# Kernel tuning notes

Hardware: AMD Instinct MI355X
Metric: run time of the kernel (lower is better)

Reference implementation:

```python
import jax, jax.numpy as jnp
import numpy as np


def _hilbert_envelope(x1d):
    """|analytic signal| of a real 1-D signal, matching scipy.signal.hilbert."""
    N = x1d.shape[0]  # static at trace time
    h = np.zeros(N, dtype=np.float32)
    if N % 2 == 0:
        h[0] = 1.0
        h[N // 2] = 1.0
        h[1:N // 2] = 2.0
    else:
        h[0] = 1.0
        h[1:(N + 1) // 2] = 2.0
    Xf = jnp.fft.fft(x1d)
    analytic = jnp.fft.ifft(Xf * jnp.asarray(h))
    return jnp.abs(analytic)


def setup_inputs() -> dict:
    key = jax.random.key(0)
    B, L, D = 32, 4096, 64
    x = jax.random.normal(key, (B, L, D), dtype=jnp.float32)
    return {"x": x}


def reference(x):
    B, L, D = x.shape
    flat = x.reshape(-1)  # [B*L*D], one long signal as in the original
    up = jnp.clip(flat, 0.0, None)
    down = jnp.clip(-flat, 0.0, None)
    envelope_max = _hilbert_envelope(up).reshape(B, L, D)
    envelope_min = (-_hilbert_envelope(down)).reshape(B, L, D)
    avg_envelope = (envelope_max + envelope_min) * 0.5
    imf = x - avg_envelope
    # torch.std(dim=1, unbiased=True) -> ddof=1 over the time axis
    std_res = jnp.std(imf, axis=1, keepdims=True, ddof=1) + jnp.float32(0.01)
    return imf / std_res, avg_envelope
```

## Files before the change

kernel.cpp:

```cpp
#include <hip/hip_runtime.h>
#include <math.h>

#define NTOT 8388608
#define N1   2048
#define N2   4096
#define BB   32
#define LL   4096
#define DD   64

enum { M_NONE = 0, M_TW = 1, M_SCALE = 4 };

__device__ inline float2 cmul(float2 a, float2 b) {
    return make_float2(a.x*b.x - a.y*b.y, a.x*b.y + a.y*b.x);
}
__device__ inline float2 cmul_conj(float2 a, float2 b) {
    return make_float2(a.x*b.x + a.y*b.y, a.y*b.x - a.x*b.y);
}
__device__ inline float2 cadd(float2 a, float2 b){ return make_float2(a.x+b.x, a.y+b.y); }
__device__ inline float2 csub(float2 a, float2 b){ return make_float2(a.x-b.x, a.y-b.y); }
__device__ inline float2 mul_pi(float2 a){ return make_float2(-a.y, a.x); }
__device__ inline float2 mul_mi(float2 a){ return make_float2(a.y, -a.x); }
__device__ inline int pidx(int a){ return a + (a >> 4); }

template<bool INV>
__device__ inline void dft8(const float2* x, float2* y) {
    const float C = 0.70710678118654752f;
    float2 t0=cadd(x[0],x[4]), t1=cadd(x[1],x[5]), t2=cadd(x[2],x[6]), t3=cadd(x[3],x[7]);
    float2 u0=csub(x[0],x[4]), u1=csub(x[1],x[5]), u2=csub(x[2],x[6]), u3=csub(x[3],x[7]);
    if (!INV) {
        u1 = make_float2(C*(u1.x+u1.y), C*(u1.y-u1.x));
        u2 = mul_mi(u2);
        u3 = make_float2(C*(u3.y-u3.x), -C*(u3.x+u3.y));
    } else {
        u1 = make_float2(C*(u1.x-u1.y), C*(u1.y+u1.x));
        u2 = mul_pi(u2);
        u3 = make_float2(-C*(u3.x+u3.y), C*(u3.x-u3.y));
    }
    {
        float2 s0=cadd(t0,t2), s1=cadd(t1,t3), d0=csub(t0,t2);
        float2 d1 = INV ? mul_pi(csub(t1,t3)) : mul_mi(csub(t1,t3));
        y[0]=cadd(s0,s1); y[4]=csub(s0,s1); y[2]=cadd(d0,d1); y[6]=csub(d0,d1);
    }
    {
        float2 s0=cadd(u0,u2), s1=cadd(u1,u3), d0=csub(u0,u2);
        float2 d1 = INV ? mul_pi(csub(u1,u3)) : mul_mi(csub(u1,u3));
        y[1]=cadd(s0,s1); y[5]=csub(s0,s1); y[3]=cadd(d0,d1); y[7]=csub(d0,d1);
    }
}

template<bool INV>
__device__ inline void dft16(const float2* x, float2* y) {
    const float C  = 0.70710678118654752f;
    const float c1 = 0.92387953251128674f;
    const float s1 = 0.38268343236508977f;
    float2 e[8], o[8], E[8], O[8];
    #pragma unroll
    for (int m = 0; m < 8; ++m) { e[m] = x[2*m]; o[m] = x[2*m+1]; }
    dft8<INV>(e, E);
    dft8<INV>(o, O);
    O[1] = cmul(O[1], make_float2( c1, INV ?  s1 : -s1));
    O[2] = cmul(O[2], make_float2(  C, INV ?   C : -C ));
    O[3] = cmul(O[3], make_float2( s1, INV ?  c1 : -c1));
    O[4] = INV ? mul_pi(O[4]) : mul_mi(O[4]);
    O[5] = cmul(O[5], make_float2(-s1, INV ?  c1 : -c1));
    O[6] = cmul(O[6], make_float2( -C, INV ?   C : -C ));
    O[7] = cmul(O[7], make_float2(-c1, INV ?  s1 : -s1));
    #pragma unroll
    for (int k = 0; k < 8; ++k) {
        y[k]     = cadd(E[k], O[k]);
        y[k + 8] = csub(E[k], O[k]);
    }
}

__device__ inline void dft8_h0_inv(const float2* x, float2* y) {
    const float C = 0.70710678118654752f;
    float2 u1 = make_float2(C*(x[1].x - x[1].y), C*(x[1].y + x[1].x));
    float2 u2 = mul_pi(x[2]);
    float2 u3 = make_float2(-C*(x[3].x + x[3].y), C*(x[3].x - x[3].y));
    {
        float2 s0=cadd(x[0],x[2]), s1=cadd(x[1],x[3]), d0=csub(x[0],x[2]);
        float2 d1 = mul_pi(csub(x[1],x[3]));
        y[0]=cadd(s0,s1); y[4]=csub(s0,s1); y[2]=cadd(d0,d1); y[6]=csub(d0,d1);
    }
    {
        float2 s0=cadd(x[0],u2), s1=cadd(u1,u3), d0=csub(x[0],u2);
        float2 d1 = mul_pi(csub(u1,u3));
        y[1]=cadd(s0,s1); y[5]=csub(s0,s1); y[3]=cadd(d0,d1); y[7]=csub(d0,d1);
    }
}

template<bool INV>
__device__ inline void dft4(const float2* u, float2* y) {
    float2 s0=cadd(u[0],u[2]), s1=cadd(u[1],u[3]), d0=csub(u[0],u[2]);
    float2 d1 = INV ? mul_pi(csub(u[1],u[3])) : mul_mi(csub(u[1],u[3]));
    y[0]=cadd(s0,s1); y[2]=csub(s0,s1); y[1]=cadd(d0,d1); y[3]=csub(d0,d1);
}

template<bool INV, int SH>
__device__ inline void twiddle8(float2* y, int ps, const float2* __restrict__ T1t) {
    float2 w1 = T1t[(ps << SH) & 4095];
    float2 w2 = cmul(w1, w1);
    float2 w3 = cmul(w2, w1);
    float2 w4 = cmul(w2, w2);
    float2 w5 = cmul(w4, w1);
    float2 w6 = cmul(w3, w3);
    float2 w7 = cmul(w4, w3);
    if (!INV) {
        y[1]=cmul(y[1],w1); y[2]=cmul(y[2],w2); y[3]=cmul(y[3],w3);
        y[4]=cmul(y[4],w4); y[5]=cmul(y[5],w5); y[6]=cmul(y[6],w6); y[7]=cmul(y[7],w7);
    } else {
        y[1]=cmul_conj(y[1],w1); y[2]=cmul_conj(y[2],w2); y[3]=cmul_conj(y[3],w3);
        y[4]=cmul_conj(y[4],w4); y[5]=cmul_conj(y[5],w5); y[6]=cmul_conj(y[6],w6); y[7]=cmul_conj(y[7],w7);
    }
}

template<bool INV>
__device__ inline void twiddle16(float2* y, int ps, const float2* __restrict__ T1t) {
    float2 w[16];
    w[1] = T1t[ps & 4095];
    w[2] = cmul(w[1], w[1]);
    w[3] = cmul(w[2], w[1]);
    w[4] = cmul(w[2], w[2]);
    w[5] = cmul(w[4], w[1]);
    w[6] = cmul(w[3], w[3]);
    w[7] = cmul(w[4], w[3]);
    w[8] = cmul(w[4], w[4]);
    w[9] = cmul(w[8], w[1]);
    w[10]= cmul(w[5], w[5]);
    w[11]= cmul(w[8], w[3]);
    w[12]= cmul(w[6], w[6]);
    w[13]= cmul(w[8], w[5]);
    w[14]= cmul(w[7], w[7]);
    w[15]= cmul(w[8], w[7]);
    #pragma unroll
    for (int k = 1; k < 16; ++k)
        y[k] = INV ? cmul_conj(y[k], w[k]) : cmul(y[k], w[k]);
}

__device__ inline float2 wbig(int t, const float2* __restrict__ T1t, const float2* __restrict__ T2t) {
    return cmul(T1t[t >> 11], T2t[t & 2047]);
}

template<bool INV, int MODE>
__global__ __launch_bounds__(256) void fft4096(float2* data,
                                               const float2* __restrict__ T1t,
                                               const float2* __restrict__ T2t) {
    __shared__ float2 S[4352];
    const int t = threadIdx.x;
    const int r = blockIdx.x;
    float2* base = data + (size_t)r * 4096;

    float2 x[16], y[16];
    #pragma unroll
    for (int m = 0; m < 16; ++m) x[m] = base[t + 256*m];

    dft16<INV>(x, y);
    twiddle16<INV>(y, t, T1t);
    #pragma unroll
    for (int k = 0; k < 16; ++k) S[pidx(16*t + k)] = y[k];
    __syncthreads();
    #pragma unroll
    for (int m = 0; m < 16; ++m) x[m] = S[pidx(t + 256*m)];

    dft16<INV>(x, y);
    {
        const int q = t & 15, ps = t - q;
        twiddle16<INV>(y, ps, T1t);
        __syncthreads();
        #pragma unroll
        for (int k = 0; k < 16; ++k) S[pidx(16*ps + q + 16*k)] = y[k];
    }
    __syncthreads();
    #pragma unroll
    for (int m = 0; m < 16; ++m) x[m] = S[pidx(t + 256*m)];

    dft16<INV>(x, y);

    if (MODE == M_TW) {
        float2 wb    = wbig(r * t, T1t, T2t);
        float2 wstep = wbig(256 * r, T1t, T2t);
        #pragma unroll
        for (int k = 0; k < 16; ++k) {
            int o = t + 256*k;
            base[o] = INV ? cmul_conj(y[k], wb) : cmul(y[k], wb);
            wb = INV ? cmul_conj(wb, wstep) : cmul(wb, wstep);
        }
    } else {
        #pragma unroll
        for (int k = 0; k < 16; ++k) {
            int o = t + 256*k;
            float2 v = y[k];
            if (MODE == M_SCALE) {
                const float sc = 1.f / 8388608.f;
                v.x *= sc; v.y *= sc;
            }
            base[o] = v;
        }
    }
}

__global__ __launch_bounds__(256) void fftmid(float2* data,
                                              const float2* __restrict__ T1t,
                                              const float2* __restrict__ T2t) {
    __shared__ float2 S[2176];
    const int t = threadIdx.x;
    const int r = blockIdx.x;
    float2* base = data + (size_t)r * 2048;

    float2 x[8], y[8];
    #pragma unroll
    for (int m = 0; m < 8; ++m) x[m] = base[t + 256*m];

    #pragma unroll
    for (int st = 0; st < 3; ++st) {
        const int s = 1 << (3*st);
        const int q = t & (s - 1);
        const int ps = t - q;
        dft8<false>(x, y);
        twiddle8<false, 1>(y, ps, T1t);
        if (st) __syncthreads();
        #pragma unroll
        for (int k = 0; k < 8; ++k) S[pidx(8*ps + q + k*s)] = y[k];
        __syncthreads();
        if (st < 2) {
            #pragma unroll
            for (int m = 0; m < 8; ++m) x[m] = S[pidx(t + 256*m)];
        }
    }
    float2 xa[4], xb[4], ya[4], yb[4];
    #pragma unroll
    for (int m = 0; m < 4; ++m) {
        xa[m] = S[pidx(t + 512*m)];
        xb[m] = S[pidx(t + 256 + 512*m)];
    }
    dft4<false>(xa, ya);
    dft4<false>(xb, yb);
    {
        float2 z[4];
        float h0 = (t == 0 && r == 0) ? 1.f : 2.f;
        z[0] = make_float2(ya[0].x * h0, ya[0].y * h0);
        z[1] = make_float2(yb[0].x * 2.f, yb[0].y * 2.f);
        z[2] = make_float2(ya[1].x * 2.f, ya[1].y * 2.f);
        z[3] = make_float2(yb[1].x * 2.f, yb[1].y * 2.f);
        dft8_h0_inv(z, y);
        if (t == 0 && r == 0) {
            float2 c = ya[2];
            #pragma unroll
            for (int k = 0; k < 8; ++k) {
                if (k & 1) { y[k].x -= c.x; y[k].y -= c.y; }
                else       { y[k].x += c.x; y[k].y += c.y; }
            }
        }
    }
    twiddle8<true, 1>(y, t, T1t);
    __syncthreads();
    #pragma unroll
    for (int k = 0; k < 8; ++k) S[pidx(8*t + k)] = y[k];
    __syncthreads();
    #pragma unroll
    for (int st = 1; st < 3; ++st) {
        const int s = 1 << (3*st);
        const int q = t & (s - 1);
        const int ps = t - q;
        #pragma unroll
        for (int m = 0; m < 8; ++m) x[m] = S[pidx(t + 256*m)];
        dft8<true>(x, y);
        twiddle8<true, 1>(y, ps, T1t);
        __syncthreads();
        #pragma unroll
        for (int k = 0; k < 8; ++k) S[pidx(8*ps + q + k*s)] = y[k];
        __syncthreads();
    }
    #pragma unroll
    for (int m = 0; m < 4; ++m) {
        xa[m] = S[pidx(t + 512*m)];
        xb[m] = S[pidx(t + 256 + 512*m)];
    }
    dft4<true>(xa, ya);
    dft4<true>(xb, yb);
    {
        float2 wka   = wbig(r * t, T1t, T2t);
        float2 w256  = wbig(256 * r, T1t, T2t);
        float2 w512  = cmul(w256, w256);
        float2 wkb   = cmul(wka, w256);
        #pragma unroll
        for (int k = 0; k < 4; ++k) {
            int o = t + 512*k;
            base[o]       = cmul_conj(ya[k], wka);
            base[o + 256] = cmul_conj(yb[k], wkb);
            wka = cmul(wka, w512);
            wkb = cmul(wkb, w512);
        }
    }
}

__global__ __launch_bounds__(256) void k_pre(const float* __restrict__ x, float2* __restrict__ A,
                                             float2* T1, float2* T2) {
    __shared__ float tile[32][33];
    int c0 = blockIdx.x * 32;
    int r0 = blockIdx.y * 32;
    int tx = threadIdx.x, ty = threadIdx.y;
    if (blockIdx.y == 0 && blockIdx.x < 24) {
        int j = blockIdx.x * 256 + ty * 32 + tx;
        if (j < 4096) {
            double ang = -2.0 * M_PI * (double)j / 4096.0;
            T1[j] = make_float2((float)cos(ang), (float)sin(ang));
        } else if (j < 4096 + 2048) {
            int b = j - 4096;
            double ang = -2.0 * M_PI * (double)b / 8388608.0;
            T2[b] = make_float2((float)cos(ang), (float)sin(ang));
        }
    }
    #pragma unroll
    for (int j = 0; j < 32; j += 8)
        tile[ty + j][tx] = x[(size_t)(r0 + ty + j) * N1 + c0 + tx];
    __syncthreads();
    #pragma unroll
    for (int j = 0; j < 32; j += 8) {
        float v = tile[tx][ty + j];
        A[(size_t)(c0 + ty + j) * N2 + r0 + tx] = make_float2(fmaxf(v, 0.f), fmaxf(-v, 0.f));
    }
}

__global__ __launch_bounds__(256) void k_trans(const float2* __restrict__ in, float2* __restrict__ out,
                                               int inCols, int inRows) {
    __shared__ float2 tile[32][33];
    int c0 = blockIdx.x * 32;
    int r0 = blockIdx.y * 32;
    int tx = threadIdx.x, ty = threadIdx.y;
    #pragma unroll
    for (int j = 0; j < 32; j += 8)
        tile[ty + j][tx] = in[(size_t)(r0 + ty + j) * inCols + c0 + tx];
    __syncthreads();
    #pragma unroll
    for (int j = 0; j < 32; j += 8)
        out[(size_t)(c0 + ty + j) * inRows + r0 + tx] = tile[tx][ty + j];
}

__global__ __launch_bounds__(256) void k_post(const float2* __restrict__ A, const float* __restrict__ x,
                                              float* __restrict__ out, float* __restrict__ part) {
    __shared__ float2 tile[32][33];
    __shared__ float red[2][8][32];
    int c0 = blockIdx.x * 32;
    int r0 = blockIdx.y * 32;
    int tx = threadIdx.x, ty = threadIdx.y;
    #pragma unroll
    for (int j = 0; j < 32; j += 8)
        tile[ty + j][tx] = A[(size_t)(r0 + ty + j) * N2 + c0 + tx];
    __syncthreads();
    float s1 = 0.f, s2 = 0.f;
    #pragma unroll
    for (int j = 0; j < 32; j += 8) {
        int n2 = c0 + ty + j;
        int n1 = r0 + tx;
        size_t n = (size_t)n2 * N1 + n1;
        float2 w = tile[tx][ty + j];
        float xv = x[n];
        float up = fmaxf(xv, 0.f);
        float dn = fmaxf(-xv, 0.f);
        float hu = w.y - dn;
        float hd = up - w.x;
        float em = sqrtf(up*up + hu*hu);
        float en = sqrtf(dn*dn + hd*hd);
        float avg = 0.5f * (em - en);
        float imf = xv - avg;
        out[NTOT + n] = avg;
        s1 += imf;
        s2 += imf * imf;
    }
    red[0][ty][tx] = s1;
    red[1][ty][tx] = s2;
    __syncthreads();
    if (ty == 0) {
        #pragma unroll
        for (int e = 1; e < 8; ++e) { s1 += red[0][e][tx]; s2 += red[1][e][tx]; }
        int slot = blockIdx.y * 128 + blockIdx.x;
        part[slot * 32 + tx]          = s1;
        part[262144 + slot * 32 + tx] = s2;
    }
}

__global__ __launch_bounds__(256) void std_final(const float* __restrict__ part, float* __restrict__ scalev) {
    int g = blockIdx.x * 256 + threadIdx.x;
    int b = g >> 6, d = g & 63;
    int dh = d >> 5, dl = d & 31;
    float s1 = 0.f, s2 = 0.f;
    for (int lq = 0; lq < 32; ++lq) {
        int by = lq * 2 + dh;
        #pragma unroll
        for (int ch = 0; ch < 4; ++ch) {
            int slot = by * 128 + b * 4 + ch;
            s1 += part[slot * 32 + dl];
            s2 += part[262144 + slot * 32 + dl];
        }
    }
    float mean = s1 / (float)LL;
    float var  = (s2 - (float)LL * mean * mean) / (float)(LL - 1);
    var = fmaxf(var, 0.f);
    scalev[g] = 1.f / (sqrtf(var) + 0.01f);
}

__global__ __launch_bounds__(256) void imf_final(const float* __restrict__ x, float* __restrict__ out,
                                                 const float* __restrict__ scalev) {
    size_t i = ((size_t)blockIdx.x * 256 + threadIdx.x) * 4;
    float4 xv = *(const float4*)(x + i);
    float4 av = *(const float4*)(out + NTOT + i);
    int b = (int)(i >> 18);
    int d = (int)(i & 63);
    const float* sc = scalev + b * 64;
    float4 v;
    v.x = (xv.x - av.x) * sc[d];
    v.y = (xv.y - av.y) * sc[d + 1];
    v.z = (xv.z - av.z) * sc[d + 2];
    v.w = (xv.w - av.w) * sc[d + 3];
    *(float4*)(out + i) = v;
}

extern "C" void kernel_launch(void* const* d_in, const int* in_sizes, int n_in,
                              void* d_out, int out_size, void* d_ws, size_t ws_size,
                              hipStream_t stream) {
    const float* x = (const float*)d_in[0];
    float* out = (float*)d_out;
    char* w = (char*)d_ws;

    float2* T1     = (float2*)w;
    float2* T2     = (float2*)(w + 32 * 1024);
    float*  scalev = (float*)(w + 48 * 1024);
    float2* A      = (float2*)(w + (1 << 20));
    float2* Bbuf   = (float2*)d_out;
    float*  part   = (float*)d_out;

    hipLaunchKernelGGL(k_pre, dim3(N1/32, N2/32), dim3(32, 8), 0, stream, x, A, T1, T2);
    hipLaunchKernelGGL((fft4096<false, M_TW>), dim3(N1), dim3(256), 0, stream, A, T1, T2);
    hipLaunchKernelGGL(k_trans, dim3(N2/32, N1/32), dim3(32, 8), 0, stream, A, Bbuf, N2, N1);
    hipLaunchKernelGGL(fftmid, dim3(N2), dim3(256), 0, stream, Bbuf, T1, T2);
    hipLaunchKernelGGL(k_trans, dim3(N1/32, N2/32), dim3(32, 8), 0, stream, Bbuf, A, N1, N2);
    hipLaunchKernelGGL((fft4096<true, M_SCALE>), dim3(N1), dim3(256), 0, stream, A, T1, T2);

    hipLaunchKernelGGL(k_post, dim3(N2/32, N1/32), dim3(32, 8), 0, stream, A, x, out, part);
    hipLaunchKernelGGL(std_final, dim3(8), dim3(256), 0, stream, part, scalev);
    hipLaunchKernelGGL(imf_final, dim3(NTOT / 4 / 256), dim3(256), 0, stream, x, out, scalev);
}
```

Baseline: 197.6 us.

## Restructure fftmid as radix-16x16x8 with 128 threads per block

The 2048-point middle FFT (forward, Hilbert mask, inverse) is rewritten from three radix-8 passes plus a radix-4 pass using 256 threads, to two radix-16 passes plus a radix-8 pass using 128 threads. Each thread now holds 16 elements, and the Hilbert-mask stage uses a new 16-point half-spectrum inverse butterfly. This removes a shared-memory exchange round and its barriers in each direction. In exchange it raises register pressure and halves the threads per block, which may reduce occupancy or latency hiding.

New measurement: 195.3 us. Within noise of the previous version (-1.2%).

```diff
diff --git a/kernel.cpp b/kernel.cpp
--- a/kernel.cpp
+++ b/kernel.cpp
@@ -86,6 +86,29 @@
         float2 s0=cadd(x[0],u2), s1=cadd(u1,u3), d0=csub(x[0],u2);
         float2 d1 = mul_pi(csub(u1,u3));
         y[1]=cadd(s0,s1); y[5]=csub(s0,s1); y[3]=cadd(d0,d1); y[7]=csub(d0,d1);
+    }
+}
+
+__device__ inline void dft16_h0_inv(const float2* x, float2* y) {
+    const float C  = 0.70710678118654752f;
+    const float c1 = 0.92387953251128674f;
+    const float s1 = 0.38268343236508977f;
+    float2 e4[4] = { x[0], x[2], x[4], x[6] };
+    float2 o4[4] = { x[1], x[3], x[5], x[7] };
+    float2 E[8], O[8];
+    dft8_h0_inv(e4, E);
+    dft8_h0_inv(o4, O);
+    O[1] = cmul(O[1], make_float2( c1,  s1));
+    O[2] = cmul(O[2], make_float2(  C,   C));
+    O[3] = cmul(O[3], make_float2( s1,  c1));
+    O[4] = mul_pi(O[4]);
+    O[5] = cmul(O[5], make_float2(-s1,  c1));
+    O[6] = cmul(O[6], make_float2( -C,   C));
+    O[7] = cmul(O[7], make_float2(-c1,  s1));
+    #pragma unroll
+    for (int k = 0; k < 8; ++k) {
+        y[k]     = cadd(E[k], O[k]);
+        y[k + 8] = csub(E[k], O[k]);
     }
 }
 
@@ -114,10 +137,10 @@
     }
 }
 
-template<bool INV>
+template<bool INV, int SH>
 __device__ inline void twiddle16(float2* y, int ps, const float2* __restrict__ T1t) {
     float2 w[16];
-    w[1] = T1t[ps & 4095];
+    w[1] = T1t[(ps << SH) & 4095];
     w[2] = cmul(w[1], w[1]);
     w[3] = cmul(w[2], w[1]);
     w[4] = cmul(w[2], w[2]);
@@ -155,7 +178,7 @@
     for (int m = 0; m < 16; ++m) x[m] = base[t + 256*m];
 
     dft16<INV>(x, y);
-    twiddle16<INV>(y, t, T1t);
+    twiddle16<INV, 0>(y, t, T1t);
     #pragma unroll
     for (int k = 0; k < 16; ++k) S[pidx(16*t + k)] = y[k];
     __syncthreads();
@@ -165,7 +188,7 @@
     dft16<INV>(x, y);
     {
         const int q = t & 15, ps = t - q;
-        twiddle16<INV>(y, ps, T1t);
+        twiddle16<INV, 0>(y, ps, T1t);
         __syncthreads();
         #pragma unroll
         for (int k = 0; k < 16; ++k) S[pidx(16*ps + q + 16*k)] = y[k];
@@ -199,7 +222,7 @@
     }
 }
 
-__global__ __launch_bounds__(256) void fftmid(float2* data,
+__global__ __launch_bounds__(128) void fftmid(float2* data,
                                               const float2* __restrict__ T1t,
                                               const float2* __restrict__ T2t) {
     __shared__ float2 S[2176];
@@ -207,89 +230,94 @@
     const int r = blockIdx.x;
     float2* base = data + (size_t)r * 2048;
 
-    float2 x[8], y[8];
-    #pragma unroll
-    for (int m = 0; m < 8; ++m) x[m] = base[t + 256*m];
-
-    #pragma unroll
-    for (int st = 0; st < 3; ++st) {
-        const int s = 1 << (3*st);
-        const int q = t & (s - 1);
-        const int ps = t - q;
-        dft8<false>(x, y);
-        twiddle8<false, 1>(y, ps, T1t);
-        if (st) __syncthreads();
-        #pragma unroll
-        for (int k = 0; k < 8; ++k) S[pidx(8*ps + q + k*s)] = y[k];
+    float2 x[16], y[16];
+    #pragma unroll
+    for (int m = 0; m < 16; ++m) x[m] = base[t + 128*m];
+
+    dft16<false>(x, y);
+    twiddle16<false, 1>(y, t, T1t);
+    #pragma unroll
+    for (int k = 0; k < 16; ++k) S[pidx(16*t + k)] = y[k];
+    __syncthreads();
+    #pragma unroll
+    for (int m = 0; m < 16; ++m) x[m] = S[pidx(t + 128*m)];
+
+    dft16<false>(x, y);
+    {
+        const int q = t & 15, ps = t - q;
+        twiddle16<false, 1>(y, ps, T1t);
         __syncthreads();
-        if (st < 2) {
-            #pragma unroll
-            for (int m = 0; m < 8; ++m) x[m] = S[pidx(t + 256*m)];
-        }
-    }
-    float2 xa[4], xb[4], ya[4], yb[4];
-    #pragma unroll
-    for (int m = 0; m < 4; ++m) {
-        xa[m] = S[pidx(t + 512*m)];
-        xb[m] = S[pidx(t + 256 + 512*m)];
-    }
-    dft4<false>(xa, ya);
-    dft4<false>(xb, yb);
-    {
-        float2 z[4];
+        #pragma unroll
+        for (int k = 0; k < 16; ++k) S[pidx(16*ps + q + 16*k)] = y[k];
+    }
+    __syncthreads();
+
+    float2 xa[8], xb[8], ya[8], yb[8];
+    #pragma unroll
+    for (int m = 0; m < 8; ++m) {
+        xa[m] = S[pidx(t + 256*m)];
+        xb[m] = S[pidx(t + 128 + 256*m)];
+    }
+    dft8<false>(xa, ya);
+    dft8<false>(xb, yb);
+    {
+        float2 z[8];
         float h0 = (t == 0 && r == 0) ? 1.f : 2.f;
-        z[0] = make_float2(ya[0].x * h0, ya[0].y * h0);
+        z[0] = make_float2(ya[0].x * h0,  ya[0].y * h0);
         z[1] = make_float2(yb[0].x * 2.f, yb[0].y * 2.f);
         z[2] = make_float2(ya[1].x * 2.f, ya[1].y * 2.f);
         z[3] = make_float2(yb[1].x * 2.f, yb[1].y * 2.f);
-        dft8_h0_inv(z, y);
+        z[4] = make_float2(ya[2].x * 2.f, ya[2].y * 2.f);
+        z[5] = make_float2(yb[2].x * 2.f, yb[2].y * 2.f);
+        z[6] = make_float2(ya[3].x * 2.f, ya[3].y * 2.f);
+        z[7] = make_float2(yb[3].x * 2.f, yb[3].y * 2.f);
+        dft16_h0_inv(z, y);
         if (t == 0 && r == 0) {
-            float2 c = ya[2];
+            float2 c = ya[4];
             #pragma unroll
-            for (int k = 0; k < 8; ++k) {
+            for (int k = 0; k < 16; ++k) {
                 if (k & 1) { y[k].x -= c.x; y[k].y -= c.y; }
                 else       { y[k].x += c.x; y[k].y += c.y; }
             }
         }
     }
-    twiddle8<true, 1>(y, t, T1t);
-    __syncthreads();
-    #pragma unroll
-    for (int k = 0; k < 8; ++k) S[pidx(8*t + k)] = y[k];
-    __syncthreads();
-    #pragma unroll
-    for (int st = 1; st < 3; ++st) {
-        const int s = 1 << (3*st);
-        const int q = t & (s - 1);
-        const int ps = t - q;
-        #pragma unroll
-        for (int m = 0; m < 8; ++m) x[m] = S[pidx(t + 256*m)];
-        dft8<true>(x, y);
-        twiddle8<true, 1>(y, ps, T1t);
+    twiddle16<true, 1>(y, t, T1t);
+    __syncthreads();
+    #pragma unroll
+    for (int k = 0; k < 16; ++k) S[pidx(16*t + k)] = y[k];
+    __syncthreads();
+
+    #pragma unroll
+    for (int m = 0; m < 16; ++m) x[m] = S[pidx(t + 128*m)];
+    dft16<true>(x, y);
+    {
+        const int q = t & 15, ps = t - q;
+        twiddle16<true, 1>(y, ps, T1t);
         __syncthreads();
         #pragma unroll
-        for (int k = 0; k < 8; ++k) S[pidx(8*ps + q + k*s)] = y[k];
-        __syncthreads();
-    }
-    #pragma unroll
-    for (int m = 0; m < 4; ++m) {
-        xa[m] = S[pidx(t + 512*m)];
-        xb[m] = S[pidx(t + 256 + 512*m)];
-    }
-    dft4<true>(xa, ya);
-    dft4<true>(xb, yb);
-    {
-        float2 wka   = wbig(r * t, T1t, T2t);
-        float2 w256  = wbig(256 * r, T1t, T2t);
-        float2 w512  = cmul(w256, w256);
-        float2 wkb   = cmul(wka, w256);
-        #pragma unroll
-        for (int k = 0; k < 4; ++k) {
-            int o = t + 512*k;
+        for (int k = 0; k < 16; ++k) S[pidx(16*ps + q + 16*k)] = y[k];
+    }
+    __syncthreads();
+
+    #pragma unroll
+    for (int m = 0; m < 8; ++m) {
+        xa[m] = S[pidx(t + 256*m)];
+        xb[m] = S[pidx(t + 128 + 256*m)];
+    }
+    dft8<true>(xa, ya);
+    dft8<true>(xb, yb);
+    {
+        float2 wka  = wbig(r * t, T1t, T2t);
+        float2 w128 = wbig(128 * r, T1t, T2t);
+        float2 w256 = cmul(w128, w128);
+        float2 wkb  = cmul(wka, w128);
+        #pragma unroll
+        for (int k = 0; k < 8; ++k) {
+            int o = t + 256*k;
             base[o]       = cmul_conj(ya[k], wka);
-            base[o + 256] = cmul_conj(yb[k], wkb);
-            wka = cmul(wka, w512);
-            wkb = cmul(wkb, w512);
+            base[o + 128] = cmul_conj(yb[k], wkb);
+            wka = cmul(wka, w256);
+            wkb = cmul(wkb, w256);
         }
     }
 }
@@ -433,7 +461,7 @@
     hipLaunchKernelGGL(k_pre, dim3(N1/32, N2/32), dim3(32, 8), 0, stream, x, A, T1, T2);
     hipLaunchKernelGGL((fft4096<false, M_TW>), dim3(N1), dim3(256), 0, stream, A, T1, T2);
     hipLaunchKernelGGL(k_trans, dim3(N2/32, N1/32), dim3(32, 8), 0, stream, A, Bbuf, N2, N1);
-    hipLaunchKernelGGL(fftmid, dim3(N2), dim3(256), 0, stream, Bbuf, T1, T2);
+    hipLaunchKernelGGL(fftmid, dim3(N2), dim3(128), 0, stream, Bbuf, T1, T2);
     hipLaunchKernelGGL(k_trans, dim3(N1/32, N2/32), dim3(32, 8), 0, stream, Bbuf, A, N1, N2);
     hipLaunchKernelGGL((fft4096<true, M_SCALE>), dim3(N1), dim3(256), 0, stream, A, T1, T2);
 
```
